# Kernel optimization log

Hardware: AMD Instinct MI355X
Metric: run time of the kernel (lower is better)

Reference implementation:

```python
import jax, jax.numpy as jnp
import numpy as np

N_NODES = 100000
N_EDGES = 1000000
N_REL = 7
IN_CH, HID_CH, OUT_CH = 128, 64, 2
N_BASES = 4  # used as num_blocks in layer 1, num_bases in layer 2


def setup_inputs() -> dict:
    key = jax.random.key(0)
    ks = jax.random.split(key, 10)
    x = jax.random.normal(ks[0], (N_NODES, IN_CH), dtype=jnp.float32)
    edge_index = jax.random.randint(ks[1], (2, N_EDGES), 0, N_NODES)
    edge_type = jax.random.randint(ks[2], (N_EDGES,), 0, N_REL)
    s = 0.05
    # layer 1: block-diagonal decomposition W1[r] is block-diag with B blocks
    W1 = jax.random.normal(ks[3], (N_REL, N_BASES, IN_CH // N_BASES, HID_CH // N_BASES), dtype=jnp.float32) * s
    root1 = jax.random.normal(ks[4], (IN_CH, HID_CH), dtype=jnp.float32) * s
    bias1 = jax.random.normal(ks[5], (HID_CH,), dtype=jnp.float32) * s
    # layer 2: basis decomposition W2[r] = sum_b comp2[r,b] * basis2[b]
    comp2 = jax.random.normal(ks[6], (N_REL, N_BASES), dtype=jnp.float32) * s
    basis2 = jax.random.normal(ks[7], (N_BASES, HID_CH, OUT_CH), dtype=jnp.float32) * s
    root2 = jax.random.normal(ks[8], (HID_CH, OUT_CH), dtype=jnp.float32) * s
    bias2 = jax.random.normal(ks[9], (OUT_CH,), dtype=jnp.float32) * s
    return {"x": x, "edge_index": edge_index, "edge_type": edge_type,
            "W1": W1, "root1": root1, "bias1": bias1,
            "comp2": comp2, "basis2": basis2, "root2": root2, "bias2": bias2}


def _relation_max_agg(msg, dst, edge_type, r, n_nodes):
    # segment-max over edges of relation r; empty segments -> 0 (PyG scatter-max behavior)
    seg = jnp.where(edge_type == r, dst, n_nodes)  # dump other relations into slot N
    agg = jax.ops.segment_max(msg, seg, num_segments=n_nodes + 1)[:n_nodes]
    deg = jax.ops.segment_sum(jnp.ones_like(seg, dtype=jnp.int32), seg, num_segments=n_nodes + 1)[:n_nodes]
    return jnp.where(deg[:, None] > 0, agg, 0.0)


def rgcn_conv_blocks(x, src, dst, edge_type, W, root, bias, n_nodes):
    # W: [R, B, in/B, out/B]  (block-diagonal weights)
    R, B, di, do = W.shape
    xb = x[src].reshape(-1, B, di)  # [E, B, in/B]
    out = x @ root + bias
    for r in range(R):
        msg = jnp.einsum('ebi,bio->ebo', xb, W[r]).reshape(-1, B * do)  # [E, out]
        out = out + _relation_max_agg(msg, dst, edge_type, r, n_nodes)
    return out


def rgcn_conv_bases(x, src, dst, edge_type, comp, basis, root, bias, n_nodes):
    # W[r] = sum_b comp[r,b] * basis[b]; basis: [B, in, out]
    W = jnp.einsum('rb,bio->rio', comp, basis)  # [R, in, out]
    xs = x[src]  # [E, in]
    out = x @ root + bias
    for r in range(W.shape[0]):
        msg = xs @ W[r]  # [E, out]
        out = out + _relation_max_agg(msg, dst, edge_type, r, n_nodes)
    return out


def reference(x, edge_index, edge_type, W1, root1, bias1, comp2, basis2, root2, bias2):
    src, dst = edge_index[0], edge_index[1]
    n = x.shape[0]
    h = rgcn_conv_blocks(x, src, dst, edge_type, W1, root1, bias1, n)
    h = jax.nn.relu(h)
    # dropout p=0.4 is identity in eval mode
    out = rgcn_conv_bases(h, src, dst, edge_type, comp2, basis2, root2, bias2, n)
    return out
```

## Files before the change

kernel.cpp:

```cpp
#include <hip/hip_runtime.h>

#define N_NODES 100000
#define N_EDGESV 1000000
#define N_REL 7
#define IN_CH 128
#define HID_CH 64
#define NBINS 800000
#define OFFM 0x0FFFFFFFu
#define NTILES 6250
#define GSTRIDE 520
#define NSB 196
#define SBCAP 8192
#define NBLK_A1 512
#define CHUNK 1954

typedef _Float16 f16;
typedef __attribute__((ext_vector_type(8))) _Float16 f16x8;
typedef __attribute__((ext_vector_type(4))) _Float16 f16x4;
typedef __attribute__((ext_vector_type(4))) float f32x4;

__global__ __launch_bounds__(256)
void passA1_kernel(const int* __restrict__ ei, const int* __restrict__ et,
                   int* __restrict__ gcur, int2* __restrict__ btmp) {
    __shared__ int2 ent[CHUNK];
    __shared__ int lhist[NSB], lcur[NSB], gposl[NSB];
    const int cbase = blockIdx.x * CHUNK;
    const int cnt = min(CHUNK, N_EDGESV - cbase);

    for (int i = threadIdx.x; i < NSB; i += 256) { lhist[i] = 0; lcur[i] = 0; }
    __syncthreads();

    for (int i = threadIdx.x; i < cnt; i += 256) {
        int e = cbase + i;
        int d = ei[N_EDGESV + e];
        int s = ei[e];
        int r = et[e];
        ent[i] = make_int2((d << 3) + r, (s * 1024 + 128 + r * 128) | (r << 28));
        atomicAdd(&lhist[d >> 9], 1);
    }
    __syncthreads();

    for (int b = threadIdx.x; b < NSB; b += 256)
        gposl[b] = atomicAdd(&gcur[b], lhist[b]);
    __syncthreads();

    for (int i = threadIdx.x; i < cnt; i += 256) {
        int2 en = ent[i];
        int b = en.x >> 12;
        int off = atomicAdd(&lcur[b], 1);
        int idx = gposl[b] + off;
        if (idx < SBCAP) btmp[(size_t)b * SBCAP + idx] = en;
    }
}

__global__ void bucketscan_kernel(const int* __restrict__ gcur, int* __restrict__ gbase,
                                  int* __restrict__ off2) {
    __shared__ int lds[256];
    int t = threadIdx.x;
    int v = (t < NSB) ? min(gcur[t], SBCAP) : 0;
    lds[t] = v;
    __syncthreads();
    for (int d = 1; d < 256; d <<= 1) {
        int x = (t >= d) ? lds[t - d] : 0;
        __syncthreads();
        if (t >= d) lds[t] += x;
        __syncthreads();
    }
    if (t < NSB) gbase[t] = lds[t] - v;
    if (t == 0) off2[0] = 0;
}

__global__ __launch_bounds__(256)
void passA2_kernel(const int* __restrict__ gcur, const int* __restrict__ gbase,
                   const int2* __restrict__ btmp, int* __restrict__ off2,
                   int* __restrict__ packed1) {
    __shared__ int hist[4096];
    __shared__ int aux[256];
    const int b = blockIdx.x >> 2;
    const int q = blockIdx.x & 3;
    const int t = threadIdx.x;
    const int cnt = min(gcur[b], SBCAP);
    const int2* base = btmp + (size_t)b * SBCAP;
    const int gb = gbase[b];

    for (int i = t; i < 4096; i += 256) hist[i] = 0;
    __syncthreads();
    for (int i = t; i < cnt; i += 256) atomicAdd(&hist[base[i].x & 4095], 1);
    __syncthreads();

    int loc[16];
    int run = 0;
#pragma unroll
    for (int j = 0; j < 16; ++j) { loc[j] = run; run += hist[t * 16 + j]; }
    aux[t] = run;
    __syncthreads();
    for (int d = 1; d < 256; d <<= 1) {
        int x = (t >= d) ? aux[t - d] : 0;
        __syncthreads();
        if (t >= d) aux[t] += x;
        __syncthreads();
    }
    const int tbase = aux[t] - run;
    __syncthreads();

#pragma unroll
    for (int j = 0; j < 16; ++j) {
        int bin = t * 16 + j;
        int excl = tbase + loc[j];
        int incl = excl + hist[bin];
        if ((t >> 6) == q) {
            int gkey = (b << 12) + bin;
            if (gkey < NBINS) off2[gkey + 1] = gb + incl;
        }
        hist[bin] = excl;
    }
    __syncthreads();

    for (int i = t; i < cnt; i += 256) {
        int2 e = base[i];
        int lb = e.x & 4095;
        if ((lb >> 10) == q) {
            int pos = gb + atomicAdd(&hist[lb], 1);
            packed1[pos] = e.y;
        }
    }
}

__global__ __launch_bounds__(256)
void xh_kernel(const float* __restrict__ x, f16* __restrict__ xh) {
    int i = blockIdx.x * blockDim.x + threadIdx.x;
    if (i < N_NODES * IN_CH / 4) {
        float4 v = ((const float4*)x)[i];
        f16x4 o = {(f16)v.x, (f16)v.y, (f16)v.z, (f16)v.w};
        *(f16x4*)(xh + (size_t)i * 4) = o;
    }
}

__global__ void wbuild_kernel(const float* __restrict__ root1, const float* __restrict__ W1,
                              const float* __restrict__ comp2, const float* __restrict__ basis2,
                              const float* __restrict__ root2, f16* __restrict__ wbt,
                              f16* __restrict__ w2t) {
    for (int idx = blockIdx.x * blockDim.x + threadIdx.x; idx < 512 * 128;
         idx += gridDim.x * blockDim.x) {
        int col = idx >> 7, k = idx & 127;
        float v;
        if (col < 64) {
            v = root1[k * HID_CH + col];
        } else {
            int cc = col - 64, r = cc >> 6, inner = cc & 63, b = inner >> 4, j = inner & 15;
            int kb = k - b * 32;
            v = (kb >= 0 && kb < 32) ? W1[(((r * 4 + b) * 32) + kb) * 16 + j] : 0.f;
        }
        wbt[idx] = (f16)v;
    }
    for (int idx = blockIdx.x * blockDim.x + threadIdx.x; idx < 16 * 64;
         idx += gridDim.x * blockDim.x) {
        int col = idx >> 6, k = idx & 63;
        float v;
        if (col < 14) {
            int r = col >> 1, oc = col & 1;
            v = 0.f;
            for (int b = 0; b < 4; ++b) v += comp2[r * 4 + b] * basis2[(b * 64 + k) * 2 + oc];
        } else {
            v = root2[k * 2 + (col - 14)];
        }
        w2t[idx] = (f16)v;
    }
}

__global__ __launch_bounds__(512, 2)
void gemm1_kernel(const f16* __restrict__ xh, const f16* __restrict__ wbt,
                  f16* __restrict__ dense1) {
    __shared__ f16 cbuf[16 * GSTRIDE];
    const int lane = threadIdx.x & 63;
    const int wv = threadIdx.x >> 6;
    const int m = lane & 15;
    const int quad = lane >> 4;

    f16x8 bf[4][4];
#pragma unroll
    for (int t = 0; t < 4; ++t) {
        const f16* wc = wbt + (size_t)(wv * 64 + t * 16 + m) * 128 + quad * 8;
#pragma unroll
        for (int kk = 0; kk < 4; ++kk)
            bf[t][kk] = *(const f16x8*)(wc + kk * 32);
    }

    int tile = blockIdx.x;
    f16x8 a[4];
    if (tile < NTILES) {
        const f16* xrow = xh + (size_t)(tile * 16 + m) * 128 + quad * 8;
#pragma unroll
        for (int kk = 0; kk < 4; ++kk) a[kk] = *(const f16x8*)(xrow + kk * 32);
    }

    while (tile < NTILES) {
        const int n0 = tile * 16;
        const int next = tile + gridDim.x;

#pragma unroll
        for (int t = 0; t < 4; ++t) {
            f32x4 acc = {0.f, 0.f, 0.f, 0.f};
#pragma unroll
            for (int kk = 0; kk < 4; ++kk)
                acc = __builtin_amdgcn_mfma_f32_16x16x32_f16(a[kk], bf[t][kk], acc, 0, 0, 0);
            const int col = wv * 64 + t * 16 + m;
#pragma unroll
            for (int i = 0; i < 4; ++i)
                cbuf[(quad * 4 + i) * GSTRIDE + col] = (f16)acc[i];
        }

        if (next < NTILES) {
            const f16* xrow = xh + (size_t)(next * 16 + m) * 128 + quad * 8;
#pragma unroll
            for (int kk = 0; kk < 4; ++kk) a[kk] = *(const f16x8*)(xrow + kk * 32);
        }

        __syncthreads();
#pragma unroll
        for (int rr = 0; rr < 2; ++rr) {
            const int row = wv * 2 + rr;
            f16x8 v = *(const f16x8*)(cbuf + row * GSTRIDE + lane * 8);
            *(f16x8*)(dense1 + (size_t)(n0 + row) * 512 + lane * 8) = v;
        }
        __syncthreads();
        tile = next;
    }
}

__global__ __launch_bounds__(256)
void agg1_kernel(const f16* __restrict__ dense1, const float* __restrict__ bias1,
                 const int* __restrict__ off2, const int* __restrict__ packed1,
                 f16* __restrict__ h16)
{
    const int lane = threadIdx.x & 63;
    const int lane2 = lane * 2;
    const char* m1 = (const char*)dense1;
    const int wid = blockIdx.x * 4 + (threadIdx.x >> 6);
    const int nw = gridDim.x * 4;
    const float bias = bias1[lane];

    for (int n = wid; n < N_NODES; n += nw) {
        const int st = off2[n << 3];
        const int en = off2[(n << 3) + 7];
        float add = 0.f, cur = 0.f;
        int prev_r = -1;

#define MRG(kk, vv) { \
        int r_ = (int)((kk) >> 28); \
        bool same_ = (r_ == prev_r); \
        add += same_ ? 0.f : cur; \
        cur = same_ ? fmaxf(cur, (vv)) : (vv); \
        prev_r = r_; }

        int p = st;
        for (; p + 3 < en; p += 4) {
            unsigned k0 = (unsigned)packed1[p];
            unsigned k1 = (unsigned)packed1[p + 1];
            unsigned k2 = (unsigned)packed1[p + 2];
            unsigned k3 = (unsigned)packed1[p + 3];
            float v0 = (float)*(const f16*)(m1 + (k0 & OFFM) + lane2);
            float v1 = (float)*(const f16*)(m1 + (k1 & OFFM) + lane2);
            float v2 = (float)*(const f16*)(m1 + (k2 & OFFM) + lane2);
            float v3 = (float)*(const f16*)(m1 + (k3 & OFFM) + lane2);
            MRG(k0, v0) MRG(k1, v1) MRG(k2, v2) MRG(k3, v3)
        }
        for (; p < en; ++p) {
            unsigned k0 = (unsigned)packed1[p];
            float v0 = (float)*(const f16*)(m1 + (k0 & OFFM) + lane2);
            MRG(k0, v0)
        }
#undef MRG
        add += cur;

        const float hroot = (float)dense1[(size_t)n * 512 + lane];
        h16[((size_t)n << 6) + lane] = (f16)fmaxf(hroot + bias + add, 0.f);
    }
}

__global__ __launch_bounds__(256)
void pre2_kernel(const f16* __restrict__ h16, const f16* __restrict__ w2t,
                 const float* __restrict__ bias2, float* __restrict__ msg2) {
    const int lane = threadIdx.x & 63;
    const int wv = threadIdx.x >> 6;
    const int nt = blockIdx.x * 4 + wv;
    if (nt >= NTILES) return;
    const int n0 = nt * 16;
    const int m = lane & 15;
    const int quad = lane >> 4;

    const f16* hrow = h16 + (size_t)(n0 + m) * 64 + quad * 8;
    const f16* wcol = w2t + (size_t)m * 64 + quad * 8;
    f32x4 acc = {0.f, 0.f, 0.f, 0.f};
    f16x8 a0 = *(const f16x8*)(hrow);
    f16x8 b0 = *(const f16x8*)(wcol);
    acc = __builtin_amdgcn_mfma_f32_16x16x32_f16(a0, b0, acc, 0, 0, 0);
    f16x8 a1 = *(const f16x8*)(hrow + 32);
    f16x8 b1 = *(const f16x8*)(wcol + 32);
    acc = __builtin_amdgcn_mfma_f32_16x16x32_f16(a1, b1, acc, 0, 0, 0);

    const float badd = (m == 14) ? bias2[0] : ((m == 15) ? bias2[1] : 0.f);
#pragma unroll
    for (int i = 0; i < 4; ++i)
        msg2[(size_t)(n0 + quad * 4 + i) * 16 + m] = acc[i] + badd;
}

__global__ __launch_bounds__(256)
void agg2_kernel(const float* __restrict__ msg2, const int* __restrict__ off2,
                 const int* __restrict__ packed1, float* __restrict__ out)
{
    const int n = blockIdx.x * blockDim.x + threadIdx.x;
    if (n >= N_NODES) return;
    const char* m2 = (const char*)msg2;
    const int st = off2[n << 3];
    const int en = off2[(n << 3) + 7];
    float addx = 0.f, addy = 0.f, curx = 0.f, cury = 0.f;
    int prev_r = -1;

#define MRG2(kk, ff) { \
    int r_ = (int)((kk) >> 28); \
    bool same_ = (r_ == prev_r); \
    addx += same_ ? 0.f : curx; \
    addy += same_ ? 0.f : cury; \
    curx = same_ ? fmaxf(curx, (ff).x) : (ff).x; \
    cury = same_ ? fmaxf(cury, (ff).y) : (ff).y; \
    prev_r = r_; }

    int p = st;
    for (; p + 1 < en; p += 2) {
        unsigned k0 = (unsigned)packed1[p], k1 = (unsigned)packed1[p + 1];
        float2 f0 = *(const float2*)(m2 + (((k0 & OFFM) >> 4) - 8));
        float2 f1 = *(const float2*)(m2 + (((k1 & OFFM) >> 4) - 8));
        MRG2(k0, f0) MRG2(k1, f1)
    }
    if (p < en) {
        unsigned k0 = (unsigned)packed1[p];
        float2 f0 = *(const float2*)(m2 + (((k0 & OFFM) >> 4) - 8));
        MRG2(k0, f0)
    }
#undef MRG2

    out[(size_t)n * 2 + 0] = msg2[(size_t)n * 16 + 14] + addx + curx;
    out[(size_t)n * 2 + 1] = msg2[(size_t)n * 16 + 15] + addy + cury;
}

extern "C" void kernel_launch(void* const* d_in, const int* in_sizes, int n_in,
                              void* d_out, int out_size, void* d_ws, size_t ws_size,
                              hipStream_t stream)
{
    const float* x      = (const float*)d_in[0];
    const int*   ei     = (const int*)d_in[1];
    const int*   et     = (const int*)d_in[2];
    const float* W1     = (const float*)d_in[3];
    const float* root1  = (const float*)d_in[4];
    const float* bias1  = (const float*)d_in[5];
    const float* comp2  = (const float*)d_in[6];
    const float* basis2 = (const float*)d_in[7];
    const float* root2  = (const float*)d_in[8];
    const float* bias2  = (const float*)d_in[9];
    float* out = (float*)d_out;

    char* ws = (char*)d_ws;
    size_t o = 0;
    auto carve = [&](size_t bytes) { char* p = ws + o; o += (bytes + 255) & ~(size_t)255; return p; };
    int*   off2    = (int*)carve(sizeof(int) * (NBINS + 1));
    int*   gcur    = (int*)carve(sizeof(int) * NSB);
    int*   gbase   = (int*)carve(sizeof(int) * NSB);
    int2*  btmp    = (int2*)carve(sizeof(int2) * (size_t)NSB * SBCAP);
    int*   packed1 = (int*)carve(sizeof(int) * N_EDGESV);
    f16*   xh      = (f16*)carve(sizeof(f16) * (size_t)N_NODES * IN_CH);
    f16*   wbt     = (f16*)carve(sizeof(f16) * 512 * 128);
    f16*   w2t     = (f16*)carve(sizeof(f16) * 16 * 64);
    f16*   dense1  = (f16*)carve(sizeof(f16) * (size_t)N_NODES * 512);
    f16*   h16     = (f16*)carve(sizeof(f16) * (size_t)N_NODES * HID_CH);
    float* msg2    = (float*)carve(sizeof(float) * (size_t)N_NODES * 16);

    hipMemsetAsync(gcur, 0, sizeof(int) * NSB, stream);
    passA1_kernel<<<NBLK_A1, 256, 0, stream>>>(ei, et, gcur, btmp);
    bucketscan_kernel<<<1, 256, 0, stream>>>(gcur, gbase, off2);
    passA2_kernel<<<NSB * 4, 256, 0, stream>>>(gcur, gbase, btmp, off2, packed1);

    xh_kernel<<<(N_NODES * IN_CH / 4 + 255) / 256, 256, 0, stream>>>(x, xh);
    wbuild_kernel<<<64, 256, 0, stream>>>(root1, W1, comp2, basis2, root2, wbt, w2t);
    gemm1_kernel<<<1024, 512, 0, stream>>>(xh, wbt, dense1);

    agg1_kernel<<<2048, 256, 0, stream>>>(dense1, bias1, off2, packed1, h16);

    pre2_kernel<<<(NTILES + 3) / 4, 256, 0, stream>>>(h16, w2t, bias2, msg2);
    agg2_kernel<<<(N_NODES + 255) / 256, 256, 0, stream>>>(msg2, off2, packed1, out);
}
```

Baseline: 280.1 us.

## Fuse fp16 conversion into GEMM, drop LDS staging, deepen gather unrolling

Removes the separate x-to-fp16 conversion kernel and its intermediate buffer; the GEMM now loads fp32 rows directly and converts them in registers. The weight matrix columns are permuted so the swapped MFMA operand order lets each lane write 16 contiguous output halves directly, which eliminates the shared-memory staging buffer and both block barriers, and occupancy is raised to 3 blocks. The gcur memset is folded into wbuild_kernel to cut one launch. The aggregation loops are unrolled further (8-way in agg1, 4-way in agg2) and the root load is hoisted, giving more loads in flight at the cost of higher register pressure.

```diff
diff --git a/kernel.cpp b/kernel.cpp
--- a/kernel.cpp
+++ b/kernel.cpp
@@ -8,7 +8,6 @@
 #define NBINS 800000
 #define OFFM 0x0FFFFFFFu
 #define NTILES 6250
-#define GSTRIDE 520
 #define NSB 196
 #define SBCAP 8192
 #define NBLK_A1 512
@@ -126,23 +125,19 @@
     }
 }
 
-__global__ __launch_bounds__(256)
-void xh_kernel(const float* __restrict__ x, f16* __restrict__ xh) {
-    int i = blockIdx.x * blockDim.x + threadIdx.x;
-    if (i < N_NODES * IN_CH / 4) {
-        float4 v = ((const float4*)x)[i];
-        f16x4 o = {(f16)v.x, (f16)v.y, (f16)v.z, (f16)v.w};
-        *(f16x4*)(xh + (size_t)i * 4) = o;
-    }
-}
-
 __global__ void wbuild_kernel(const float* __restrict__ root1, const float* __restrict__ W1,
                               const float* __restrict__ comp2, const float* __restrict__ basis2,
                               const float* __restrict__ root2, f16* __restrict__ wbt,
-                              f16* __restrict__ w2t) {
+                              f16* __restrict__ w2t, int* __restrict__ gcur) {
+    if (blockIdx.x == 0) {
+        for (int i = threadIdx.x; i < NSB; i += 256) gcur[i] = 0;
+    }
     for (int idx = blockIdx.x * blockDim.x + threadIdx.x; idx < 512 * 128;
          idx += gridDim.x * blockDim.x) {
-        int col = idx >> 7, k = idx & 127;
+        int p = idx >> 7, k = idx & 127;
+        int lp = p & 63;
+        int lc = ((lp & 15) >> 2) * 16 + ((lp >> 4) << 2) + (lp & 3);
+        int col = (p & ~63) | lc;
         float v;
         if (col < 64) {
             v = root1[k * HID_CH + col];
@@ -168,10 +163,9 @@
     }
 }
 
-__global__ __launch_bounds__(512, 2)
-void gemm1_kernel(const f16* __restrict__ xh, const f16* __restrict__ wbt,
+__global__ __launch_bounds__(512, 3)
+void gemm1_kernel(const float* __restrict__ x, const f16* __restrict__ wbt,
                   f16* __restrict__ dense1) {
-    __shared__ f16 cbuf[16 * GSTRIDE];
     const int lane = threadIdx.x & 63;
     const int wv = threadIdx.x >> 6;
     const int m = lane & 15;
@@ -187,43 +181,53 @@
     }
 
     int tile = blockIdx.x;
-    f16x8 a[4];
+    float4 xa[8];
     if (tile < NTILES) {
-        const f16* xrow = xh + (size_t)(tile * 16 + m) * 128 + quad * 8;
-#pragma unroll
-        for (int kk = 0; kk < 4; ++kk) a[kk] = *(const f16x8*)(xrow + kk * 32);
+        const float* xr = x + (size_t)(tile * 16 + m) * 128 + quad * 8;
+#pragma unroll
+        for (int kk = 0; kk < 4; ++kk) {
+            xa[kk * 2]     = *(const float4*)(xr + kk * 32);
+            xa[kk * 2 + 1] = *(const float4*)(xr + kk * 32 + 4);
+        }
     }
 
     while (tile < NTILES) {
         const int n0 = tile * 16;
         const int next = tile + gridDim.x;
 
+        f16x8 a[4];
+#pragma unroll
+        for (int kk = 0; kk < 4; ++kk) {
+            float4 lo = xa[kk * 2], hi = xa[kk * 2 + 1];
+            f16x8 t8 = {(f16)lo.x, (f16)lo.y, (f16)lo.z, (f16)lo.w,
+                        (f16)hi.x, (f16)hi.y, (f16)hi.z, (f16)hi.w};
+            a[kk] = t8;
+        }
+
+        if (next < NTILES) {
+            const float* xr = x + (size_t)(next * 16 + m) * 128 + quad * 8;
+#pragma unroll
+            for (int kk = 0; kk < 4; ++kk) {
+                xa[kk * 2]     = *(const float4*)(xr + kk * 32);
+                xa[kk * 2 + 1] = *(const float4*)(xr + kk * 32 + 4);
+            }
+        }
+
+        f16x8 hv[2];
 #pragma unroll
         for (int t = 0; t < 4; ++t) {
             f32x4 acc = {0.f, 0.f, 0.f, 0.f};
 #pragma unroll
             for (int kk = 0; kk < 4; ++kk)
-                acc = __builtin_amdgcn_mfma_f32_16x16x32_f16(a[kk], bf[t][kk], acc, 0, 0, 0);
-            const int col = wv * 64 + t * 16 + m;
+                acc = __builtin_amdgcn_mfma_f32_16x16x32_f16(bf[t][kk], a[kk], acc, 0, 0, 0);
 #pragma unroll
             for (int i = 0; i < 4; ++i)
-                cbuf[(quad * 4 + i) * GSTRIDE + col] = (f16)acc[i];
-        }
-
-        if (next < NTILES) {
-            const f16* xrow = xh + (size_t)(next * 16 + m) * 128 + quad * 8;
-#pragma unroll
-            for (int kk = 0; kk < 4; ++kk) a[kk] = *(const f16x8*)(xrow + kk * 32);
-        }
-
-        __syncthreads();
-#pragma unroll
-        for (int rr = 0; rr < 2; ++rr) {
-            const int row = wv * 2 + rr;
-            f16x8 v = *(const f16x8*)(cbuf + row * GSTRIDE + lane * 8);
-            *(f16x8*)(dense1 + (size_t)(n0 + row) * 512 + lane * 8) = v;
-        }
-        __syncthreads();
+                hv[t >> 1][(t & 1) * 4 + i] = (f16)acc[i];
+        }
+
+        f16* dst = dense1 + (size_t)(n0 + m) * 512 + wv * 64 + quad * 16;
+        *(f16x8*)dst       = hv[0];
+        *(f16x8*)(dst + 8) = hv[1];
         tile = next;
     }
 }
@@ -243,6 +247,7 @@
     for (int n = wid; n < N_NODES; n += nw) {
         const int st = off2[n << 3];
         const int en = off2[(n << 3) + 7];
+        const float hroot = (float)dense1[(size_t)n * 512 + lane];
         float add = 0.f, cur = 0.f;
         int prev_r = -1;
 
@@ -254,6 +259,26 @@
         prev_r = r_; }
 
         int p = st;
+        for (; p + 7 < en; p += 8) {
+            unsigned k0 = (unsigned)packed1[p];
+            unsigned k1 = (unsigned)packed1[p + 1];
+            unsigned k2 = (unsigned)packed1[p + 2];
+            unsigned k3 = (unsigned)packed1[p + 3];
+            unsigned k4 = (unsigned)packed1[p + 4];
+            unsigned k5 = (unsigned)packed1[p + 5];
+            unsigned k6 = (unsigned)packed1[p + 6];
+            unsigned k7 = (unsigned)packed1[p + 7];
+            float v0 = (float)*(const f16*)(m1 + (k0 & OFFM) + lane2);
+            float v1 = (float)*(const f16*)(m1 + (k1 & OFFM) + lane2);
+            float v2 = (float)*(const f16*)(m1 + (k2 & OFFM) + lane2);
+            float v3 = (float)*(const f16*)(m1 + (k3 & OFFM) + lane2);
+            float v4 = (float)*(const f16*)(m1 + (k4 & OFFM) + lane2);
+            float v5 = (float)*(const f16*)(m1 + (k5 & OFFM) + lane2);
+            float v6 = (float)*(const f16*)(m1 + (k6 & OFFM) + lane2);
+            float v7 = (float)*(const f16*)(m1 + (k7 & OFFM) + lane2);
+            MRG(k0, v0) MRG(k1, v1) MRG(k2, v2) MRG(k3, v3)
+            MRG(k4, v4) MRG(k5, v5) MRG(k6, v6) MRG(k7, v7)
+        }
         for (; p + 3 < en; p += 4) {
             unsigned k0 = (unsigned)packed1[p];
             unsigned k1 = (unsigned)packed1[p + 1];
@@ -273,7 +298,6 @@
 #undef MRG
         add += cur;
 
-        const float hroot = (float)dense1[(size_t)n * 512 + lane];
         h16[((size_t)n << 6) + lane] = (f16)fmaxf(hroot + bias + add, 0.f);
     }
 }
@@ -327,13 +351,16 @@
     prev_r = r_; }
 
     int p = st;
-    for (; p + 1 < en; p += 2) {
+    for (; p + 3 < en; p += 4) {
         unsigned k0 = (unsigned)packed1[p], k1 = (unsigned)packed1[p + 1];
+        unsigned k2 = (unsigned)packed1[p + 2], k3 = (unsigned)packed1[p + 3];
         float2 f0 = *(const float2*)(m2 + (((k0 & OFFM) >> 4) - 8));
         float2 f1 = *(const float2*)(m2 + (((k1 & OFFM) >> 4) - 8));
-        MRG2(k0, f0) MRG2(k1, f1)
-    }
-    if (p < en) {
+        float2 f2 = *(const float2*)(m2 + (((k2 & OFFM) >> 4) - 8));
+        float2 f3 = *(const float2*)(m2 + (((k3 & OFFM) >> 4) - 8));
+        MRG2(k0, f0) MRG2(k1, f1) MRG2(k2, f2) MRG2(k3, f3)
+    }
+    for (; p < en; ++p) {
         unsigned k0 = (unsigned)packed1[p];
         float2 f0 = *(const float2*)(m2 + (((k0 & OFFM) >> 4) - 8));
         MRG2(k0, f0)
@@ -368,21 +395,19 @@
     int*   gbase   = (int*)carve(sizeof(int) * NSB);
     int2*  btmp    = (int2*)carve(sizeof(int2) * (size_t)NSB * SBCAP);
     int*   packed1 = (int*)carve(sizeof(int) * N_EDGESV);
-    f16*   xh      = (f16*)carve(sizeof(f16) * (size_t)N_NODES * IN_CH);
     f16*   wbt     = (f16*)carve(sizeof(f16) * 512 * 128);
     f16*   w2t     = (f16*)carve(sizeof(f16) * 16 * 64);
     f16*   dense1  = (f16*)carve(sizeof(f16) * (size_t)N_NODES * 512);
     f16*   h16     = (f16*)carve(sizeof(f16) * (size_t)N_NODES * HID_CH);
     float* msg2    = (float*)carve(sizeof(float) * (size_t)N_NODES * 16);
 
-    hipMemsetAsync(gcur, 0, sizeof(int) * NSB, stream);
+    wbuild_kernel<<<64, 256, 0, stream>>>(root1, W1, comp2, basis2, root2, wbt, w2t, gcur);
+
     passA1_kernel<<<NBLK_A1, 256, 0, stream>>>(ei, et, gcur, btmp);
     bucketscan_kernel<<<1, 256, 0, stream>>>(gcur, gbase, off2);
     passA2_kernel<<<NSB * 4, 256, 0, stream>>>(gcur, gbase, btmp, off2, packed1);
 
-    xh_kernel<<<(N_NODES * IN_CH / 4 + 255) / 256, 256, 0, stream>>>(x, xh);
-    wbuild_kernel<<<64, 256, 0, stream>>>(root1, W1, comp2, basis2, root2, wbt, w2t);
-    gemm1_kernel<<<1024, 512, 0, stream>>>(xh, wbt, dense1);
+    gemm1_kernel<<<1024, 512, 0, stream>>>(x, wbt, dense1);
 
     agg1_kernel<<<2048, 256, 0, stream>>>(dense1, bias1, off2, packed1, h16);
 
```

Measured after the change: 283.2 us. No clear change (+1.1%).

## Fuse preprocessing kernels into two launches and deepen gather unrolling

Applied to the files above, without the earlier changes.

Merges edge bucketing, fp32-to-fp16 conversion and weight building into one heterogeneous launch. The bucket scan, second sort pass and first GEMM are merged into another launch whose sort blocks are interleaved with GEMM blocks; each sort block recomputes the bucket prefix sum instead of reading it from a separate scan kernel. This cuts four launches and lets independent work overlap on the device. It also unrolls the edge gather loops in both aggregation kernels to eight and hoists the root load in agg1 to expose more memory parallelism. In exchange it adds redundant scans per block and larger, divergent fused kernels.

```diff
diff --git a/kernel.cpp b/kernel.cpp
--- a/kernel.cpp
+++ b/kernel.cpp
@@ -13,6 +13,11 @@
 #define SBCAP 8192
 #define NBLK_A1 512
 #define CHUNK 1954
+#define XH_BLOCKS 2048
+#define WB_BLOCKS 64
+#define XH_TOTAL (N_NODES * IN_CH / 4)
+#define GEMM_BLOCKS 1024
+#define NBLK_A2 (NSB * 4)
 
 typedef _Float16 f16;
 typedef __attribute__((ext_vector_type(8))) _Float16 f16x8;
@@ -20,211 +25,218 @@
 typedef __attribute__((ext_vector_type(4))) float f32x4;
 
 __global__ __launch_bounds__(256)
-void passA1_kernel(const int* __restrict__ ei, const int* __restrict__ et,
-                   int* __restrict__ gcur, int2* __restrict__ btmp) {
+void k1_fused_kernel(const int* __restrict__ ei, const int* __restrict__ et,
+                     int* __restrict__ gcur, int2* __restrict__ btmp,
+                     const float* __restrict__ x, f16* __restrict__ xh,
+                     const float* __restrict__ root1, const float* __restrict__ W1,
+                     const float* __restrict__ comp2, const float* __restrict__ basis2,
+                     const float* __restrict__ root2, f16* __restrict__ wbt,
+                     f16* __restrict__ w2t)
+{
     __shared__ int2 ent[CHUNK];
     __shared__ int lhist[NSB], lcur[NSB], gposl[NSB];
-    const int cbase = blockIdx.x * CHUNK;
-    const int cnt = min(CHUNK, N_EDGESV - cbase);
-
-    for (int i = threadIdx.x; i < NSB; i += 256) { lhist[i] = 0; lcur[i] = 0; }
-    __syncthreads();
-
-    for (int i = threadIdx.x; i < cnt; i += 256) {
-        int e = cbase + i;
-        int d = ei[N_EDGESV + e];
-        int s = ei[e];
-        int r = et[e];
-        ent[i] = make_int2((d << 3) + r, (s * 1024 + 128 + r * 128) | (r << 28));
-        atomicAdd(&lhist[d >> 9], 1);
+    const int bid = blockIdx.x;
+
+    if (bid < NBLK_A1) {
+        const int cbase = bid * CHUNK;
+        const int cnt = min(CHUNK, N_EDGESV - cbase);
+
+        for (int i = threadIdx.x; i < NSB; i += 256) { lhist[i] = 0; lcur[i] = 0; }
+        __syncthreads();
+
+        for (int i = threadIdx.x; i < cnt; i += 256) {
+            int e = cbase + i;
+            int d = ei[N_EDGESV + e];
+            int s = ei[e];
+            int r = et[e];
+            ent[i] = make_int2((d << 3) + r, (s * 1024 + 128 + r * 128) | (r << 28));
+            atomicAdd(&lhist[d >> 9], 1);
+        }
+        __syncthreads();
+
+        for (int b = threadIdx.x; b < NSB; b += 256)
+            gposl[b] = atomicAdd(&gcur[b], lhist[b]);
+        __syncthreads();
+
+        for (int i = threadIdx.x; i < cnt; i += 256) {
+            int2 en = ent[i];
+            int b = en.x >> 12;
+            int off = atomicAdd(&lcur[b], 1);
+            int idx = gposl[b] + off;
+            if (idx < SBCAP) btmp[(size_t)b * SBCAP + idx] = en;
+        }
+    } else if (bid < NBLK_A1 + XH_BLOCKS) {
+        for (int i = (bid - NBLK_A1) * 256 + threadIdx.x; i < XH_TOTAL;
+             i += XH_BLOCKS * 256) {
+            float4 v = ((const float4*)x)[i];
+            f16x4 o = {(f16)v.x, (f16)v.y, (f16)v.z, (f16)v.w};
+            *(f16x4*)(xh + (size_t)i * 4) = o;
+        }
+    } else {
+        const int t0 = (bid - NBLK_A1 - XH_BLOCKS) * 256 + threadIdx.x;
+        for (int idx = t0; idx < 512 * 128; idx += WB_BLOCKS * 256) {
+            int col = idx >> 7, k = idx & 127;
+            float v;
+            if (col < 64) {
+                v = root1[k * HID_CH + col];
+            } else {
+                int cc = col - 64, r = cc >> 6, inner = cc & 63, b = inner >> 4, j = inner & 15;
+                int kb = k - b * 32;
+                v = (kb >= 0 && kb < 32) ? W1[(((r * 4 + b) * 32) + kb) * 16 + j] : 0.f;
+            }
+            wbt[idx] = (f16)v;
+        }
+        for (int idx = t0; idx < 16 * 64; idx += WB_BLOCKS * 256) {
+            int col = idx >> 6, k = idx & 63;
+            float v;
+            if (col < 14) {
+                int r = col >> 1, oc = col & 1;
+                v = 0.f;
+                for (int b = 0; b < 4; ++b) v += comp2[r * 4 + b] * basis2[(b * 64 + k) * 2 + oc];
+            } else {
+                v = root2[k * 2 + (col - 14)];
+            }
+            w2t[idx] = (f16)v;
+        }
     }
-    __syncthreads();
-
-    for (int b = threadIdx.x; b < NSB; b += 256)
-        gposl[b] = atomicAdd(&gcur[b], lhist[b]);
-    __syncthreads();
-
-    for (int i = threadIdx.x; i < cnt; i += 256) {
-        int2 en = ent[i];
-        int b = en.x >> 12;
-        int off = atomicAdd(&lcur[b], 1);
-        int idx = gposl[b] + off;
-        if (idx < SBCAP) btmp[(size_t)b * SBCAP + idx] = en;
-    }
-}
-
-__global__ void bucketscan_kernel(const int* __restrict__ gcur, int* __restrict__ gbase,
-                                  int* __restrict__ off2) {
-    __shared__ int lds[256];
-    int t = threadIdx.x;
-    int v = (t < NSB) ? min(gcur[t], SBCAP) : 0;
-    lds[t] = v;
-    __syncthreads();
-    for (int d = 1; d < 256; d <<= 1) {
-        int x = (t >= d) ? lds[t - d] : 0;
-        __syncthreads();
-        if (t >= d) lds[t] += x;
-        __syncthreads();
-    }
-    if (t < NSB) gbase[t] = lds[t] - v;
-    if (t == 0) off2[0] = 0;
-}
-
-__global__ __launch_bounds__(256)
-void passA2_kernel(const int* __restrict__ gcur, const int* __restrict__ gbase,
-                   const int2* __restrict__ btmp, int* __restrict__ off2,
-                   int* __restrict__ packed1) {
-    __shared__ int hist[4096];
-    __shared__ int aux[256];
-    const int b = blockIdx.x >> 2;
-    const int q = blockIdx.x & 3;
-    const int t = threadIdx.x;
-    const int cnt = min(gcur[b], SBCAP);
-    const int2* base = btmp + (size_t)b * SBCAP;
-    const int gb = gbase[b];
-
-    for (int i = t; i < 4096; i += 256) hist[i] = 0;
-    __syncthreads();
-    for (int i = t; i < cnt; i += 256) atomicAdd(&hist[base[i].x & 4095], 1);
-    __syncthreads();
-
-    int loc[16];
-    int run = 0;
-#pragma unroll
-    for (int j = 0; j < 16; ++j) { loc[j] = run; run += hist[t * 16 + j]; }
-    aux[t] = run;
-    __syncthreads();
-    for (int d = 1; d < 256; d <<= 1) {
-        int x = (t >= d) ? aux[t - d] : 0;
-        __syncthreads();
-        if (t >= d) aux[t] += x;
-        __syncthreads();
-    }
-    const int tbase = aux[t] - run;
-    __syncthreads();
-
-#pragma unroll
-    for (int j = 0; j < 16; ++j) {
-        int bin = t * 16 + j;
-        int excl = tbase + loc[j];
-        int incl = excl + hist[bin];
-        if ((t >> 6) == q) {
-            int gkey = (b << 12) + bin;
-            if (gkey < NBINS) off2[gkey + 1] = gb + incl;
-        }
-        hist[bin] = excl;
-    }
-    __syncthreads();
-
-    for (int i = t; i < cnt; i += 256) {
-        int2 e = base[i];
-        int lb = e.x & 4095;
-        if ((lb >> 10) == q) {
-            int pos = gb + atomicAdd(&hist[lb], 1);
-            packed1[pos] = e.y;
-        }
-    }
-}
-
-__global__ __launch_bounds__(256)
-void xh_kernel(const float* __restrict__ x, f16* __restrict__ xh) {
-    int i = blockIdx.x * blockDim.x + threadIdx.x;
-    if (i < N_NODES * IN_CH / 4) {
-        float4 v = ((const float4*)x)[i];
-        f16x4 o = {(f16)v.x, (f16)v.y, (f16)v.z, (f16)v.w};
-        *(f16x4*)(xh + (size_t)i * 4) = o;
-    }
-}
-
-__global__ void wbuild_kernel(const float* __restrict__ root1, const float* __restrict__ W1,
-                              const float* __restrict__ comp2, const float* __restrict__ basis2,
-                              const float* __restrict__ root2, f16* __restrict__ wbt,
-                              f16* __restrict__ w2t) {
-    for (int idx = blockIdx.x * blockDim.x + threadIdx.x; idx < 512 * 128;
-         idx += gridDim.x * blockDim.x) {
-        int col = idx >> 7, k = idx & 127;
-        float v;
-        if (col < 64) {
-            v = root1[k * HID_CH + col];
-        } else {
-            int cc = col - 64, r = cc >> 6, inner = cc & 63, b = inner >> 4, j = inner & 15;
-            int kb = k - b * 32;
-            v = (kb >= 0 && kb < 32) ? W1[(((r * 4 + b) * 32) + kb) * 16 + j] : 0.f;
-        }
-        wbt[idx] = (f16)v;
-    }
-    for (int idx = blockIdx.x * blockDim.x + threadIdx.x; idx < 16 * 64;
-         idx += gridDim.x * blockDim.x) {
-        int col = idx >> 6, k = idx & 63;
-        float v;
-        if (col < 14) {
-            int r = col >> 1, oc = col & 1;
-            v = 0.f;
-            for (int b = 0; b < 4; ++b) v += comp2[r * 4 + b] * basis2[(b * 64 + k) * 2 + oc];
-        } else {
-            v = root2[k * 2 + (col - 14)];
-        }
-        w2t[idx] = (f16)v;
-    }
 }
 
 __global__ __launch_bounds__(512, 2)
-void gemm1_kernel(const f16* __restrict__ xh, const f16* __restrict__ wbt,
-                  f16* __restrict__ dense1) {
-    __shared__ f16 cbuf[16 * GSTRIDE];
-    const int lane = threadIdx.x & 63;
-    const int wv = threadIdx.x >> 6;
-    const int m = lane & 15;
-    const int quad = lane >> 4;
-
-    f16x8 bf[4][4];
-#pragma unroll
-    for (int t = 0; t < 4; ++t) {
-        const f16* wc = wbt + (size_t)(wv * 64 + t * 16 + m) * 128 + quad * 8;
-#pragma unroll
-        for (int kk = 0; kk < 4; ++kk)
-            bf[t][kk] = *(const f16x8*)(wc + kk * 32);
-    }
-
-    int tile = blockIdx.x;
-    f16x8 a[4];
-    if (tile < NTILES) {
-        const f16* xrow = xh + (size_t)(tile * 16 + m) * 128 + quad * 8;
-#pragma unroll
-        for (int kk = 0; kk < 4; ++kk) a[kk] = *(const f16x8*)(xrow + kk * 32);
-    }
-
-    while (tile < NTILES) {
-        const int n0 = tile * 16;
-        const int next = tile + gridDim.x;
-
+void k3_fused_kernel(const f16* __restrict__ xh, const f16* __restrict__ wbt,
+                     f16* __restrict__ dense1,
+                     const int* __restrict__ gcur, const int2* __restrict__ btmp,
+                     int* __restrict__ off2, int* __restrict__ packed1)
+{
+    __shared__ __align__(16) char smem[18448];
+
+    const int bid = blockIdx.x;
+    int rid; bool is_a2;
+    if (bid < 2 * NBLK_A2) { is_a2 = (bid & 1); rid = bid >> 1; }
+    else { is_a2 = false; rid = NBLK_A2 + (bid - 2 * NBLK_A2); }
+
+    if (!is_a2) {
+        f16* cbuf = (f16*)smem;
+        const int lane = threadIdx.x & 63;
+        const int wv = threadIdx.x >> 6;
+        const int m = lane & 15;
+        const int quad = lane >> 4;
+
+        f16x8 bf[4][4];
 #pragma unroll
         for (int t = 0; t < 4; ++t) {
-            f32x4 acc = {0.f, 0.f, 0.f, 0.f};
+            const f16* wc = wbt + (size_t)(wv * 64 + t * 16 + m) * 128 + quad * 8;
 #pragma unroll
             for (int kk = 0; kk < 4; ++kk)
-                acc = __builtin_amdgcn_mfma_f32_16x16x32_f16(a[kk], bf[t][kk], acc, 0, 0, 0);
-            const int col = wv * 64 + t * 16 + m;
-#pragma unroll
-            for (int i = 0; i < 4; ++i)
-                cbuf[(quad * 4 + i) * GSTRIDE + col] = (f16)acc[i];
-        }
-
-        if (next < NTILES) {
-            const f16* xrow = xh + (size_t)(next * 16 + m) * 128 + quad * 8;
+                bf[t][kk] = *(const f16x8*)(wc + kk * 32);
+        }
+
+        int tile = rid;
+        f16x8 a[4];
+        if (tile < NTILES) {
+            const f16* xrow = xh + (size_t)(tile * 16 + m) * 128 + quad * 8;
 #pragma unroll
             for (int kk = 0; kk < 4; ++kk) a[kk] = *(const f16x8*)(xrow + kk * 32);
         }
 
-        __syncthreads();
-#pragma unroll
-        for (int rr = 0; rr < 2; ++rr) {
-            const int row = wv * 2 + rr;
-            f16x8 v = *(const f16x8*)(cbuf + row * GSTRIDE + lane * 8);
-            *(f16x8*)(dense1 + (size_t)(n0 + row) * 512 + lane * 8) = v;
-        }
-        __syncthreads();
-        tile = next;
+        while (tile < NTILES) {
+            const int n0 = tile * 16;
+            const int next = tile + GEMM_BLOCKS;
+
+#pragma unroll
+            for (int t = 0; t < 4; ++t) {
+                f32x4 acc = {0.f, 0.f, 0.f, 0.f};
+#pragma unroll
+                for (int kk = 0; kk < 4; ++kk)
+                    acc = __builtin_amdgcn_mfma_f32_16x16x32_f16(a[kk], bf[t][kk], acc, 0, 0, 0);
+                const int col = wv * 64 + t * 16 + m;
+#pragma unroll
+                for (int i = 0; i < 4; ++i)
+                    cbuf[(quad * 4 + i) * GSTRIDE + col] = (f16)acc[i];
+            }
+
+            if (next < NTILES) {
+                const f16* xrow = xh + (size_t)(next * 16 + m) * 128 + quad * 8;
+#pragma unroll
+                for (int kk = 0; kk < 4; ++kk) a[kk] = *(const f16x8*)(xrow + kk * 32);
+            }
+
+            __syncthreads();
+#pragma unroll
+            for (int rr = 0; rr < 2; ++rr) {
+                const int row = wv * 2 + rr;
+                f16x8 v = *(const f16x8*)(cbuf + row * GSTRIDE + lane * 8);
+                *(f16x8*)(dense1 + (size_t)(n0 + row) * 512 + lane * 8) = v;
+            }
+            __syncthreads();
+            tile = next;
+        }
+    } else {
+        int* hist = (int*)smem;
+        int* aux  = (int*)(smem + 16384);
+        int* shv  = (int*)(smem + 18432);
+        const int b = rid >> 2;
+        const int q = rid & 3;
+        const int t = threadIdx.x;
+
+        if (rid == 0 && t == 0) off2[0] = 0;
+
+        int v = (t < NSB) ? min(gcur[t], SBCAP) : 0;
+        aux[t] = v;
+        __syncthreads();
+        for (int d = 1; d < 256; d <<= 1) {
+            int xv = (t >= d) ? aux[t - d] : 0;
+            __syncthreads();
+            if (t >= d) aux[t] += xv;
+            __syncthreads();
+        }
+        if (t == 0) shv[0] = (b == 0) ? 0 : aux[b - 1];
+        __syncthreads();
+        const int gb = shv[0];
+        const int cnt = min(gcur[b], SBCAP);
+        const int2* base = btmp + (size_t)b * SBCAP;
+        __syncthreads();
+
+        for (int i = t; i < 4096; i += 512) hist[i] = 0;
+        __syncthreads();
+        for (int i = t; i < cnt; i += 512) atomicAdd(&hist[base[i].x & 4095], 1);
+        __syncthreads();
+
+        int loc[8];
+        int run = 0;
+#pragma unroll
+        for (int j = 0; j < 8; ++j) { loc[j] = run; run += hist[t * 8 + j]; }
+        aux[t] = run;
+        __syncthreads();
+        for (int d = 1; d < 512; d <<= 1) {
+            int xv = (t >= d) ? aux[t - d] : 0;
+            __syncthreads();
+            if (t >= d) aux[t] += xv;
+            __syncthreads();
+        }
+        const int tbase = aux[t] - run;
+        __syncthreads();
+
+#pragma unroll
+        for (int j = 0; j < 8; ++j) {
+            int bin = t * 8 + j;
+            int excl = tbase + loc[j];
+            int incl = excl + hist[bin];
+            if ((t >> 7) == q) {
+                int gkey = (b << 12) + bin;
+                if (gkey < NBINS) off2[gkey + 1] = gb + incl;
+            }
+            hist[bin] = excl;
+        }
+        __syncthreads();
+
+        for (int i = t; i < cnt; i += 512) {
+            int2 e = base[i];
+            int lb = e.x & 4095;
+            if ((lb >> 10) == q) {
+                int pos = gb + atomicAdd(&hist[lb], 1);
+                packed1[pos] = e.y;
+            }
+        }
     }
 }
 
@@ -243,6 +255,7 @@
     for (int n = wid; n < N_NODES; n += nw) {
         const int st = off2[n << 3];
         const int en = off2[(n << 3) + 7];
+        const float hroot = (float)dense1[(size_t)n * 512 + lane];
         float add = 0.f, cur = 0.f;
         int prev_r = -1;
 
@@ -254,6 +267,26 @@
         prev_r = r_; }
 
         int p = st;
+        for (; p + 7 < en; p += 8) {
+            unsigned k0 = (unsigned)packed1[p];
+            unsigned k1 = (unsigned)packed1[p + 1];
+            unsigned k2 = (unsigned)packed1[p + 2];
+            unsigned k3 = (unsigned)packed1[p + 3];
+            unsigned k4 = (unsigned)packed1[p + 4];
+            unsigned k5 = (unsigned)packed1[p + 5];
+            unsigned k6 = (unsigned)packed1[p + 6];
+            unsigned k7 = (unsigned)packed1[p + 7];
+            float v0 = (float)*(const f16*)(m1 + (k0 & OFFM) + lane2);
+            float v1 = (float)*(const f16*)(m1 + (k1 & OFFM) + lane2);
+            float v2 = (float)*(const f16*)(m1 + (k2 & OFFM) + lane2);
+            float v3 = (float)*(const f16*)(m1 + (k3 & OFFM) + lane2);
+            float v4 = (float)*(const f16*)(m1 + (k4 & OFFM) + lane2);
+            float v5 = (float)*(const f16*)(m1 + (k5 & OFFM) + lane2);
+            float v6 = (float)*(const f16*)(m1 + (k6 & OFFM) + lane2);
+            float v7 = (float)*(const f16*)(m1 + (k7 & OFFM) + lane2);
+            MRG(k0, v0) MRG(k1, v1) MRG(k2, v2) MRG(k3, v3)
+            MRG(k4, v4) MRG(k5, v5) MRG(k6, v6) MRG(k7, v7)
+        }
         for (; p + 3 < en; p += 4) {
             unsigned k0 = (unsigned)packed1[p];
             unsigned k1 = (unsigned)packed1[p + 1];
@@ -273,7 +306,6 @@
 #undef MRG
         add += cur;
 
-        const float hroot = (float)dense1[(size_t)n * 512 + lane];
         h16[((size_t)n << 6) + lane] = (f16)fmaxf(hroot + bias + add, 0.f);
     }
 }
@@ -327,13 +359,23 @@
     prev_r = r_; }
 
     int p = st;
-    for (; p + 1 < en; p += 2) {
-        unsigned k0 = (unsigned)packed1[p], k1 = (unsigned)packed1[p + 1];
+    for (; p + 7 < en; p += 8) {
+        unsigned k0 = (unsigned)packed1[p],     k1 = (unsigned)packed1[p + 1];
+        unsigned k2 = (unsigned)packed1[p + 2], k3 = (unsigned)packed1[p + 3];
+        unsigned k4 = (unsigned)packed1[p + 4], k5 = (unsigned)packed1[p + 5];
+        unsigned k6 = (unsigned)packed1[p + 6], k7 = (unsigned)packed1[p + 7];
         float2 f0 = *(const float2*)(m2 + (((k0 & OFFM) >> 4) - 8));
         float2 f1 = *(const float2*)(m2 + (((k1 & OFFM) >> 4) - 8));
-        MRG2(k0, f0) MRG2(k1, f1)
+        float2 f2 = *(const float2*)(m2 + (((k2 & OFFM) >> 4) - 8));
+        float2 f3 = *(const float2*)(m2 + (((k3 & OFFM) >> 4) - 8));
+        float2 f4 = *(const float2*)(m2 + (((k4 & OFFM) >> 4) - 8));
+        float2 f5 = *(const float2*)(m2 + (((k5 & OFFM) >> 4) - 8));
+        float2 f6 = *(const float2*)(m2 + (((k6 & OFFM) >> 4) - 8));
+        float2 f7 = *(const float2*)(m2 + (((k7 & OFFM) >> 4) - 8));
+        MRG2(k0, f0) MRG2(k1, f1) MRG2(k2, f2) MRG2(k3, f3)
+        MRG2(k4, f4) MRG2(k5, f5) MRG2(k6, f6) MRG2(k7, f7)
     }
-    if (p < en) {
+    for (; p < en; ++p) {
         unsigned k0 = (unsigned)packed1[p];
         float2 f0 = *(const float2*)(m2 + (((k0 & OFFM) >> 4) - 8));
         MRG2(k0, f0)
@@ -365,7 +407,6 @@
     auto carve = [&](size_t bytes) { char* p = ws + o; o += (bytes + 255) & ~(size_t)255; return p; };
     int*   off2    = (int*)carve(sizeof(int) * (NBINS + 1));
     int*   gcur    = (int*)carve(sizeof(int) * NSB);
-    int*   gbase   = (int*)carve(sizeof(int) * NSB);
     int2*  btmp    = (int2*)carve(sizeof(int2) * (size_t)NSB * SBCAP);
     int*   packed1 = (int*)carve(sizeof(int) * N_EDGESV);
     f16*   xh      = (f16*)carve(sizeof(f16) * (size_t)N_NODES * IN_CH);
@@ -376,13 +417,12 @@
     float* msg2    = (float*)carve(sizeof(float) * (size_t)N_NODES * 16);
 
     hipMemsetAsync(gcur, 0, sizeof(int) * NSB, stream);
-    passA1_kernel<<<NBLK_A1, 256, 0, stream>>>(ei, et, gcur, btmp);
-    bucketscan_kernel<<<1, 256, 0, stream>>>(gcur, gbase, off2);
-    passA2_kernel<<<NSB * 4, 256, 0, stream>>>(gcur, gbase, btmp, off2, packed1);
-
-    xh_kernel<<<(N_NODES * IN_CH / 4 + 255) / 256, 256, 0, stream>>>(x, xh);
-    wbuild_kernel<<<64, 256, 0, stream>>>(root1, W1, comp2, basis2, root2, wbt, w2t);
-    gemm1_kernel<<<1024, 512, 0, stream>>>(xh, wbt, dense1);
+
+    k1_fused_kernel<<<NBLK_A1 + XH_BLOCKS + WB_BLOCKS, 256, 0, stream>>>(
+        ei, et, gcur, btmp, x, xh, root1, W1, comp2, basis2, root2, wbt, w2t);
+
+    k3_fused_kernel<<<2 * NBLK_A2 + (GEMM_BLOCKS - NBLK_A2), 512, 0, stream>>>(
+        xh, wbt, dense1, gcur, btmp, off2, packed1);
 
     agg1_kernel<<<2048, 256, 0, stream>>>(dense1, bias1, off2, packed1, h16);
 
```

Result: faster. 273.7 us (-2.3%).
